# Kernel tuning notes

Hardware: AMD Instinct MI355X
Metric: run time of the kernel (lower is better)

The kernel has to match this reference:

```python
import jax, jax.numpy as jnp
import numpy as np

N_NODES = 100000
EPS = 1e-07


def _gconv(src, dst, x, W, b):
    # DGL GraphConv with norm='both': D_dst^{-1/2} A (D_src^{-1/2} x) W + b
    ones = jnp.ones(src.shape[0], x.dtype)
    deg_out = jax.ops.segment_sum(ones, src, num_segments=N_NODES)
    deg_in = jax.ops.segment_sum(ones, dst, num_segments=N_NODES)
    norm_out = jnp.where(deg_out > 0, deg_out, 1.0) ** -0.5
    norm_in = jnp.where(deg_in > 0, deg_in, 1.0) ** -0.5
    h = x * norm_out[:, None]
    agg = jax.ops.segment_sum(h[src], dst, num_segments=N_NODES)  # [N, d]
    agg = agg * norm_in[:, None]
    return agg @ W + b


def _branch(npemb, gauss, unif, temp, Wm, bm, Wl, bl, Wq, bq, Wd1, bd1, WdX, bdX, Wc, bc):
    cat = unif.shape[-1]
    mean = npemb @ Wm + bm                      # [E, d_z]
    logstd = npemb @ Wl + bl                    # [E, d_z]
    Nlat = gauss * jnp.exp(logstd) + mean       # reparameterization
    Nlat = Nlat.reshape(npemb.shape[0], cat, -1)  # [E, cat, d_m]
    q = npemb @ Wq + bq                         # [E, cat]
    gumbel = -jnp.log(-jnp.log(unif + EPS) + EPS)
    Z = jax.nn.softmax((q + gumbel) / temp, axis=-1)  # [E, cat]
    M = jnp.einsum('ec,ecd->ed', Z, Nlat)       # [E, d_m]
    X = jax.nn.relu(jax.nn.relu(M @ Wd1 + bd1) @ WdX + bdX)
    A = jax.nn.softmax(M @ Wc + bc, axis=-1)
    return A, X, mean, logstd, q


def setup_inputs() -> dict:
    key = jax.random.key(0)
    ks = jax.random.split(key, 32)
    E_g, E = 800000, 262144
    d_in, d_h, d_z, cat, d_m, d_dec, d_out = 128, 256, 256, 4, 64, 256, 128
    s = 0.05
    inp = {
        'x': jax.random.normal(ks[0], (N_NODES, d_in), jnp.float32),
        'src': jax.random.randint(ks[1], (E_g,), 0, N_NODES),
        'dst': jax.random.randint(ks[2], (E_g,), 0, N_NODES),
        'pos_src': jax.random.randint(ks[3], (E,), 0, N_NODES),
        'pos_dst': jax.random.randint(ks[4], (E,), 0, N_NODES),
        'neg_src': jax.random.randint(ks[5], (E,), 0, N_NODES),
        'neg_dst': jax.random.randint(ks[6], (E,), 0, N_NODES),
        'gauss_pos': jax.random.normal(ks[7], (E, d_z), jnp.float32),
        'gauss_neg': jax.random.normal(ks[8], (E, d_z), jnp.float32),
        'unif_pos': jax.random.uniform(ks[9], (E, cat), jnp.float32),
        'unif_neg': jax.random.uniform(ks[10], (E, cat), jnp.float32),
        'temp': 1,
        'W1': jax.random.normal(ks[11], (d_in, d_h), jnp.float32) * s,
        'b1': jnp.zeros((d_h,), jnp.float32),
        'W2': jax.random.normal(ks[12], (d_h, d_h), jnp.float32) * s,
        'b2': jnp.zeros((d_h,), jnp.float32),
        'Wm': jax.random.normal(ks[13], (d_h, d_z), jnp.float32) * s,
        'bm': jnp.zeros((d_z,), jnp.float32),
        'Wl': jax.random.normal(ks[14], (d_h, d_z), jnp.float32) * s,
        'bl': jnp.zeros((d_z,), jnp.float32),
        'Wq': jax.random.normal(ks[15], (d_h, cat), jnp.float32) * s,
        'bq': jnp.zeros((cat,), jnp.float32),
        'Wd1': jax.random.normal(ks[16], (d_m, d_dec), jnp.float32) * s,
        'bd1': jnp.zeros((d_dec,), jnp.float32),
        'WdX': jax.random.normal(ks[17], (d_dec, d_out), jnp.float32) * s,
        'bdX': jnp.zeros((d_out,), jnp.float32),
        'Wc': jax.random.normal(ks[18], (d_m, cat), jnp.float32) * s,
        'bc': jnp.zeros((cat,), jnp.float32),
    }
    return inp


def reference(x, src, dst, pos_src, pos_dst, neg_src, neg_dst,
              gauss_pos, gauss_neg, unif_pos, unif_neg, temp,
              W1, b1, W2, b2, Wm, bm, Wl, bl, Wq, bq,
              Wd1, bd1, WdX, bdX, Wc, bc):
    # two-layer GraphConv encoder (relu after layer 0; dropout in eval mode = identity)
    h = jax.nn.relu(_gconv(src, dst, x, W1, b1))
    h = _gconv(src, dst, h, W2, b2)
    # u_add_v edge gather
    pos_npemb = h[pos_src] + h[pos_dst]
    neg_npemb = h[neg_src] + h[neg_dst]
    t = jnp.asarray(temp, h.dtype)
    posA, posX, pos_mean, pos_logstd, posq = _branch(
        pos_npemb, gauss_pos, unif_pos, t, Wm, bm, Wl, bl, Wq, bq, Wd1, bd1, WdX, bdX, Wc, bc)
    negA, negX, neg_mean, neg_logstd, negq = _branch(
        neg_npemb, gauss_neg, unif_neg, t, Wm, bm, Wl, bl, Wq, bq, Wd1, bd1, WdX, bdX, Wc, bc)
    return (posA, negA, posX, negX, pos_mean, neg_mean,
            pos_logstd, neg_logstd, posq, negq)
```

## Files before the change

kernel.cpp:

```cpp
#include <hip/hip_runtime.h>
#include <hip/hip_bf16.h>


#define NN 100000
#define EG 800000
#define EE 262144
#define NB 98

typedef __attribute__((ext_vector_type(8))) short short8;
typedef __attribute__((ext_vector_type(4))) float f32x4;
typedef __attribute__((ext_vector_type(2))) float f32x2;

__device__ __forceinline__ float lo2f(unsigned u) {
  union { unsigned u; float f; } v; v.u = u << 16; return v.f;
}
__device__ __forceinline__ float hi2f(unsigned u) {
  union { unsigned u; float f; } v; v.u = u & 0xFFFF0000u; return v.f;
}
__device__ __forceinline__ unsigned short f2bf(float f) {
  union { float f; unsigned u; } v; v.f = f;
  return (unsigned short)((v.u + 0x7FFFu + ((v.u >> 16) & 1u)) >> 16);
}
__device__ __forceinline__ unsigned pack2bf(float a, float b) {
  return (unsigned)f2bf(a) | ((unsigned)f2bf(b) << 16);
}
__device__ __forceinline__ int permc(int c) {
  return (c & ~31) | ((c & 15) << 1) | ((c >> 4) & 1);
}

__device__ __forceinline__ float decode_scalar(const void* p) {
  unsigned u = *(const unsigned*)p;
  float f = __uint_as_float(u);
  float af = fabsf(f);
  if (af >= 1e-6f && af <= 1e6f) return f;
  if (u < 1024u) return (float)u;
  return 1.0f;
}

__global__ __launch_bounds__(256) void k_deg(const int* __restrict__ src,
                                             const int* __restrict__ dst,
                                             int* __restrict__ degO,
                                             int* __restrict__ degI) {
  for (int i = blockIdx.x * 256 + threadIdx.x; i < EG; i += gridDim.x * 256) {
    atomicAdd(&degO[src[i]], 1);
    atomicAdd(&degI[dst[i]], 1);
  }
}

__global__ __launch_bounds__(1024) void k_scan1(const int* __restrict__ degI,
                                                int* __restrict__ rowptr,
                                                int* __restrict__ bsum) {
  __shared__ int wsum[16];
  int t = threadIdx.x, lane = t & 63, wv = t >> 6;
  int i = blockIdx.x * 1024 + t;
  int v = (i < NN) ? degI[i] : 0;
  int incl = v;
#pragma unroll
  for (int off = 1; off < 64; off <<= 1) {
    int u = __shfl_up(incl, off);
    if (lane >= off) incl += u;
  }
  if (lane == 63) wsum[wv] = incl;
  __syncthreads();
  if (wv == 0 && lane < 16) {
    int s = wsum[lane];
    int si = s;
#pragma unroll
    for (int off = 1; off < 16; off <<= 1) {
      int u = __shfl_up(si, off);
      if (lane >= off) si += u;
    }
    wsum[lane] = si - s;
    if (lane == 15) bsum[blockIdx.x] = si;
  }
  __syncthreads();
  int excl = wsum[wv] + incl - v;
  if (i < NN) rowptr[i] = excl;
}

__global__ __launch_bounds__(128) void k_scan2(int* __restrict__ bsum) {
  __shared__ int w0tot;
  int t = threadIdx.x, lane = t & 63, wv = t >> 6;
  int v = (t < NB) ? bsum[t] : 0;
  int incl = v;
#pragma unroll
  for (int off = 1; off < 64; off <<= 1) {
    int u = __shfl_up(incl, off);
    if (lane >= off) incl += u;
  }
  if (wv == 0 && lane == 63) w0tot = incl;
  __syncthreads();
  int excl = incl - v + (wv ? w0tot : 0);
  if (t < NB) bsum[t] = excl;
}

__global__ __launch_bounds__(1024) void k_scan3(const int* __restrict__ degI,
                                                const int* __restrict__ degO,
                                                int* __restrict__ rowptr,
                                                int* __restrict__ cursor,
                                                const int* __restrict__ bsum,
                                                float* __restrict__ normO,
                                                float* __restrict__ normI) {
  int i = blockIdx.x * 1024 + threadIdx.x;
  if (i < NN) {
    int vv = rowptr[i] + bsum[blockIdx.x];
    rowptr[i] = vv;
    cursor[i] = vv;
    if (i == NN - 1) rowptr[NN] = vv + degI[i];
    int dO = degO[i]; if (dO < 1) dO = 1;
    int dI = degI[i]; if (dI < 1) dI = 1;
    normO[i] = rsqrtf((float)dO);
    normI[i] = rsqrtf((float)dI);
  }
}

__global__ __launch_bounds__(256) void k_fill(const int* __restrict__ src,
                                              const int* __restrict__ dst,
                                              int* __restrict__ cursor,
                                              int* __restrict__ csr) {
  for (int e = blockIdx.x * 256 + threadIdx.x; e < EG; e += gridDim.x * 256) {
    int d = dst[e];
    int pos = atomicAdd(&cursor[d], 1);
    csr[pos] = src[e];
  }
}

__global__ __launch_bounds__(256) void k_transpose_all(
    const float* __restrict__ W1, const float* __restrict__ W2,
    const float* __restrict__ Wm, const float* __restrict__ Wl,
    const float* __restrict__ Wd1, const float* __restrict__ WdX,
    const float* __restrict__ Wq,
    unsigned short* __restrict__ W1T, unsigned short* __restrict__ W2T,
    unsigned short* __restrict__ WmT, unsigned short* __restrict__ WlT,
    unsigned short* __restrict__ Wd1T, unsigned short* __restrict__ WdXT,
    unsigned short* __restrict__ WqT) {
  int idx = blockIdx.x * 256 + threadIdx.x;
  if (idx < 32768) {
    int n = idx & 255, k = idx >> 8;
    W1T[n * 128 + k] = f2bf(W1[idx]);
  } else if (idx < 98304) {
    int i = idx - 32768;
    int n = i & 255, k = i >> 8;
    W2T[n * 256 + k] = f2bf(W2[i]);
  } else if (idx < 163840) {
    int i = idx - 98304;
    int n = i & 255, k = i >> 8;
    WmT[n * 256 + k] = f2bf(Wm[i]);
  } else if (idx < 229376) {
    int i = idx - 163840;
    int n = i & 255, k = i >> 8;
    WlT[n * 256 + k] = f2bf(Wl[i]);
  } else if (idx < 245760) {
    int i = idx - 229376;
    int n = i & 255, k = i >> 8;
    Wd1T[n * 64 + k] = f2bf(Wd1[i]);
  } else if (idx < 278528) {
    int i = idx - 245760;
    int n = i & 127, k = i >> 7;
    WdXT[n * 256 + k] = f2bf(WdX[i]);
  } else if (idx < 282624) {
    int i = idx - 278528;
    int r = i >> 8, k = i & 255;
    WqT[i] = (r < 4) ? f2bf(Wq[k * 4 + r]) : (unsigned short)0;
  }
}

__global__ __launch_bounds__(256) void k_gather1(
    const float* __restrict__ x, const int* __restrict__ rowptr,
    const int* __restrict__ csr, const float* __restrict__ normO,
    const float* __restrict__ normI, unsigned short* __restrict__ agg) {
  int wid = (blockIdx.x * 256 + threadIdx.x) >> 6;
  int lane = threadIdx.x & 63;
  int half = lane >> 5, fl = lane & 31;
  int nw = (gridDim.x * 256) >> 6;
  for (int n = wid; n < NN; n += nw) {
    int beg = rowptr[n], end = rowptr[n + 1];
    float a0 = 0.f, a1 = 0.f, a2 = 0.f, a3 = 0.f;
    float b0 = 0.f, b1 = 0.f, b2 = 0.f, b3 = 0.f;
    int i = beg + half;
    for (; i + 2 < end; i += 4) {
      int s0 = csr[i], s1 = csr[i + 2];
      float ns0 = normO[s0], ns1 = normO[s1];
      float4 v0 = *(const float4*)(x + ((size_t)s0 << 7) + (fl << 2));
      float4 v1 = *(const float4*)(x + ((size_t)s1 << 7) + (fl << 2));
      a0 += ns0 * v0.x; a1 += ns0 * v0.y; a2 += ns0 * v0.z; a3 += ns0 * v0.w;
      b0 += ns1 * v1.x; b1 += ns1 * v1.y; b2 += ns1 * v1.z; b3 += ns1 * v1.w;
    }
    for (; i < end; i += 2) {
      int s0 = csr[i];
      float ns0 = normO[s0];
      float4 v0 = *(const float4*)(x + ((size_t)s0 << 7) + (fl << 2));
      a0 += ns0 * v0.x; a1 += ns0 * v0.y; a2 += ns0 * v0.z; a3 += ns0 * v0.w;
    }
    a0 += b0; a1 += b1; a2 += b2; a3 += b3;
    a0 += __shfl_xor(a0, 32); a1 += __shfl_xor(a1, 32);
    a2 += __shfl_xor(a2, 32); a3 += __shfl_xor(a3, 32);
    if (lane < 32) {
      float ni = normI[n];
      *(uint2*)(agg + ((size_t)n << 7) + (fl << 2)) =
          make_uint2(pack2bf(a0 * ni, a1 * ni), pack2bf(a2 * ni, a3 * ni));
    }
  }
}

__global__ __launch_bounds__(256) void k_gather2(
    const unsigned short* __restrict__ h1s, const int* __restrict__ rowptr,
    const int* __restrict__ csr, const float* __restrict__ normI,
    unsigned short* __restrict__ agg) {
  int wid = (blockIdx.x * 256 + threadIdx.x) >> 6;
  int lane = threadIdx.x & 63;
  int half = lane >> 5, fl = lane & 31;
  int nw = (gridDim.x * 256) >> 6;
  for (int n = wid; n < NN; n += nw) {
    int beg = rowptr[n], end = rowptr[n + 1];
    float a0 = 0.f, a1 = 0.f, a2 = 0.f, a3 = 0.f, a4 = 0.f, a5 = 0.f, a6 = 0.f, a7 = 0.f;
    float c0 = 0.f, c1 = 0.f, c2 = 0.f, c3 = 0.f, c4 = 0.f, c5 = 0.f, c6 = 0.f, c7 = 0.f;
    int i = beg + half;
    for (; i + 2 < end; i += 4) {
      int s0 = csr[i], s1 = csr[i + 2];
      uint4 v = *(const uint4*)(h1s + ((size_t)s0 << 8) + (fl << 3));
      uint4 u = *(const uint4*)(h1s + ((size_t)s1 << 8) + (fl << 3));
      a0 += lo2f(v.x); a1 += hi2f(v.x);
      a2 += lo2f(v.y); a3 += hi2f(v.y);
      a4 += lo2f(v.z); a5 += hi2f(v.z);
      a6 += lo2f(v.w); a7 += hi2f(v.w);
      c0 += lo2f(u.x); c1 += hi2f(u.x);
      c2 += lo2f(u.y); c3 += hi2f(u.y);
      c4 += lo2f(u.z); c5 += hi2f(u.z);
      c6 += lo2f(u.w); c7 += hi2f(u.w);
    }
    for (; i < end; i += 2) {
      int s0 = csr[i];
      uint4 v = *(const uint4*)(h1s + ((size_t)s0 << 8) + (fl << 3));
      a0 += lo2f(v.x); a1 += hi2f(v.x);
      a2 += lo2f(v.y); a3 += hi2f(v.y);
      a4 += lo2f(v.z); a5 += hi2f(v.z);
      a6 += lo2f(v.w); a7 += hi2f(v.w);
    }
    a0 += c0; a1 += c1; a2 += c2; a3 += c3;
    a4 += c4; a5 += c5; a6 += c6; a7 += c7;
    a0 += __shfl_xor(a0, 32); a1 += __shfl_xor(a1, 32);
    a2 += __shfl_xor(a2, 32); a3 += __shfl_xor(a3, 32);
    a4 += __shfl_xor(a4, 32); a5 += __shfl_xor(a5, 32);
    a6 += __shfl_xor(a6, 32); a7 += __shfl_xor(a7, 32);
    if (lane < 32) {
      float ni = normI[n];
      uint4 o;
      o.x = pack2bf(a0 * ni, a1 * ni);
      o.y = pack2bf(a2 * ni, a3 * ni);
      o.z = pack2bf(a4 * ni, a5 * ni);
      o.w = pack2bf(a6 * ni, a7 * ni);
      *(uint4*)(agg + ((size_t)n << 8) + (fl << 3)) = o;
    }
  }
}

template <int K, bool RELU, bool OSCALE>
__global__ __launch_bounds__(256) void k_gemm(
    const unsigned short* __restrict__ A, const float* __restrict__ oscale,
    const unsigned short* __restrict__ WT, const float* __restrict__ bias,
    unsigned short* __restrict__ C, int M) {
  __shared__ __align__(16) short At[128 * 40];
  __shared__ __align__(16) short Bt[256 * 40];
  const int t = threadIdx.x;
  const int row0 = blockIdx.x * 128;
  const int lane = t & 63, wave = t >> 6;
  const int wr = (wave >> 1) << 6;
  const int wcc = (wave & 1) << 7;
  const int lrow = lane & 15, lhi = lane >> 4;

  f32x4 acc[4][8];
#pragma unroll
  for (int m = 0; m < 4; ++m)
#pragma unroll
    for (int n = 0; n < 8; ++n) acc[m][n] = (f32x4){0.f, 0.f, 0.f, 0.f};

  for (int k0 = 0; k0 < K; k0 += 32) {
    if (k0) __syncthreads();
#pragma unroll
    for (int it = 0; it < 2; ++it) {
      int idx = t + it * 256;
      int r = idx >> 2, c8 = (idx & 3) << 3;
      int grow = row0 + r;
      int4 tv = {0, 0, 0, 0};
      if (grow < M) tv = *(const int4*)(A + (size_t)grow * K + k0 + c8);
      *(int4*)&At[r * 40 + c8] = tv;
    }
    {
      const unsigned short* wt = WT + (size_t)permc(t) * K + k0;
      *(int4*)&Bt[t * 40 + 0] = *(const int4*)(wt);
      *(int4*)&Bt[t * 40 + 8] = *(const int4*)(wt + 8);
      *(int4*)&Bt[t * 40 + 16] = *(const int4*)(wt + 16);
      *(int4*)&Bt[t * 40 + 24] = *(const int4*)(wt + 24);
    }
    __syncthreads();
    short8 a[4], b[8];
#pragma unroll
    for (int m = 0; m < 4; ++m)
      a[m] = *(const short8*)&At[(wr + m * 16 + lrow) * 40 + lhi * 8];
#pragma unroll
    for (int n = 0; n < 8; ++n)
      b[n] = *(const short8*)&Bt[(wcc + n * 16 + lrow) * 40 + lhi * 8];
#pragma unroll
    for (int m = 0; m < 4; ++m)
#pragma unroll
      for (int n = 0; n < 8; ++n)
        acc[m][n] = __builtin_amdgcn_mfma_f32_16x16x32_bf16(a[m], b[n], acc[m][n], 0, 0, 0);
  }
#pragma unroll
  for (int np = 0; np < 4; ++np) {
    int tc = wcc + np * 32 + (lrow << 1);
    float bv0 = bias[tc], bv1 = bias[tc + 1];
#pragma unroll
    for (int m = 0; m < 4; ++m) {
#pragma unroll
      for (int r = 0; r < 4; ++r) {
        int grow = row0 + wr + m * 16 + lhi * 4 + r;
        if (grow < M) {
          float v0 = acc[m][2 * np][r] + bv0;
          float v1 = acc[m][2 * np + 1][r] + bv1;
          if (RELU) { v0 = fmaxf(v0, 0.f); v1 = fmaxf(v1, 0.f); }
          if (OSCALE) { float s = oscale[grow]; v0 *= s; v1 *= s; }
          *(unsigned*)&C[(size_t)grow * 256 + tc] = pack2bf(v0, v1);
        }
      }
    }
  }
}

__global__ __launch_bounds__(512) void k_branch2(
    const unsigned short* __restrict__ h, const int* __restrict__ ea,
    const int* __restrict__ eb, const float* __restrict__ gauss,
    const float* __restrict__ unif, const void* __restrict__ temp_p,
    const unsigned short* __restrict__ WmT, const float* __restrict__ bm,
    const unsigned short* __restrict__ WlT, const float* __restrict__ bl,
    const unsigned short* __restrict__ WqT, const float* __restrict__ bq,
    const float* __restrict__ Wc, const float* __restrict__ bc,
    float* __restrict__ o_mean, float* __restrict__ o_ls,
    float* __restrict__ q_o, float* __restrict__ A_o,
    unsigned* __restrict__ M_o32) {
  __shared__ __align__(16) char U[33792];
  short* At = (short*)U;
  float* Mf = (float*)U;
  __shared__ float zS[512];
  __shared__ float qS[512];
  __shared__ float WcT[4 * 68];
  __shared__ float bmS[256], blS[256];
  __shared__ int eaS[128], ebS[128];

  const int t = threadIdx.x;
  const int e0 = blockIdx.x << 7;
  const int lane = t & 63;
  const int wv = t >> 6;
  const int lrow = lane & 15, lhi = lane >> 4;
  const int wc = wv << 5;

  if (t < 256) {
    bmS[t] = bm[t]; blS[t] = bl[t];
    WcT[(t & 3) * 68 + (t >> 2)] = Wc[t];
  } else if (t < 384) {
    eaS[t - 256] = ea[e0 + t - 256];
  } else {
    ebS[t - 384] = eb[e0 + t - 384];
  }
  __syncthreads();

  f32x4 am[8][2], al[8][2], aq;
#pragma unroll
  for (int m = 0; m < 8; ++m)
#pragma unroll
    for (int n = 0; n < 2; ++n) {
      am[m][n] = (f32x4){0.f, 0.f, 0.f, 0.f};
      al[m][n] = (f32x4){0.f, 0.f, 0.f, 0.f};
    }
  aq = (f32x4){0.f, 0.f, 0.f, 0.f};

  const int ar = t >> 2, as_ = t & 3;
  const int arsw = ((as_ ^ (ar & 3)) << 3);
  const int fsw = (lrow & 3);

  const unsigned short* pa_base = h + ((size_t)eaS[ar] << 8) + (as_ << 3);
  const unsigned short* pb_base = h + ((size_t)ebS[ar] << 8) + (as_ << 3);
  const size_t row0p = (size_t)permc(wc + lrow) << 8;
  const size_t row1p = (size_t)permc(wc + 16 + lrow) << 8;
  const unsigned short* bm0p = WmT + row0p + (lhi << 3);
  const unsigned short* bm1p = WmT + row1p + (lhi << 3);
  const unsigned short* bl0p = WlT + row0p + (lhi << 3);
  const unsigned short* bl1p = WlT + row1p + (lhi << 3);
  const unsigned short* bqp = WqT + ((size_t)lrow << 8) + (lhi << 3);

  uint4 va = *(const uint4*)pa_base;
  uint4 vb = *(const uint4*)pb_base;

  for (int k0 = 0; k0 < 256; k0 += 32) {
    unsigned w0 = pack2bf(lo2f(va.x) + lo2f(vb.x), hi2f(va.x) + hi2f(vb.x));
    unsigned w1 = pack2bf(lo2f(va.y) + lo2f(vb.y), hi2f(va.y) + hi2f(vb.y));
    unsigned w2 = pack2bf(lo2f(va.z) + lo2f(vb.z), hi2f(va.z) + hi2f(vb.z));
    unsigned w3 = pack2bf(lo2f(va.w) + lo2f(vb.w), hi2f(va.w) + hi2f(vb.w));
    if (k0 < 224) {
      va = *(const uint4*)(pa_base + k0 + 32);
      vb = *(const uint4*)(pb_base + k0 + 32);
    }
    short8 bmf0 = *(const short8*)(bm0p + k0);
    short8 bmf1 = *(const short8*)(bm1p + k0);
    short8 blf0 = *(const short8*)(bl0p + k0);
    short8 blf1 = *(const short8*)(bl1p + k0);
    short8 bqf = *(const short8*)(bqp + k0);
    if (k0) __syncthreads();
    *(int4*)&At[ar * 32 + arsw] = make_int4((int)w0, (int)w1, (int)w2, (int)w3);
    __syncthreads();
    short8 a[8], aqa;
#pragma unroll
    for (int m = 0; m < 8; ++m)
      a[m] = *(const short8*)&At[(m * 16 + lrow) * 32 + ((lhi ^ fsw) << 3)];
    aqa = *(const short8*)&At[((wv << 4) + lrow) * 32 + ((lhi ^ fsw) << 3)];
#pragma unroll
    for (int m = 0; m < 8; ++m) {
      am[m][0] = __builtin_amdgcn_mfma_f32_16x16x32_bf16(a[m], bmf0, am[m][0], 0, 0, 0);
      am[m][1] = __builtin_amdgcn_mfma_f32_16x16x32_bf16(a[m], bmf1, am[m][1], 0, 0, 0);
      al[m][0] = __builtin_amdgcn_mfma_f32_16x16x32_bf16(a[m], blf0, al[m][0], 0, 0, 0);
      al[m][1] = __builtin_amdgcn_mfma_f32_16x16x32_bf16(a[m], blf1, al[m][1], 0, 0, 0);
    }
    aq = __builtin_amdgcn_mfma_f32_16x16x32_bf16(aqa, bqf, aq, 0, 0, 0);
  }
  __syncthreads();

  float invt = 1.0f / decode_scalar(temp_p);
  float qb = (lrow < 4) ? bq[lrow] : 0.f;
#pragma unroll
  for (int r = 0; r < 4; ++r) {
    int el = (wv << 4) + lhi * 4 + r;
    float q = aq[r] + qb;
    float uu = 0.5f;
    if (lrow < 4) uu = unif[(((size_t)(e0 + el)) << 2) + lrow];
    float g = -__logf(-__logf(uu + 1e-7f) + 1e-7f);
    float z = (q + g) * invt;
    float mx = fmaxf(z, __shfl_xor(z, 1));
    mx = fmaxf(mx, __shfl_xor(mx, 2));
    float ez = __expf(z - mx);
    float sz = ez + __shfl_xor(ez, 1);
    sz += __shfl_xor(sz, 2);
    if (lrow < 4) { zS[el * 4 + lrow] = ez / sz; qS[el * 4 + lrow] = q; }
  }
  for (int i = t; i < 128 * 66; i += 512) Mf[i] = 0.f;
  __syncthreads();

  __builtin_nontemporal_store(qS[t], q_o + (((size_t)e0) << 2) + t);

  const int cidx = wv >> 1;
  const int dd = ((wv & 1) << 5) + (lrow << 1);
  const int tc = wc + (lrow << 1);
  float bm0 = bmS[tc], bm1 = bmS[tc + 1];
  float bl0 = blS[tc], bl1 = blS[tc + 1];
#pragma unroll
  for (int m = 0; m < 8; ++m) {
#pragma unroll
    for (int r = 0; r < 4; ++r) {
      int row = m * 16 + lhi * 4 + r;
      size_t gi = (((size_t)(e0 + row)) << 8) + tc;
      float mv0 = am[m][0][r] + bm0, mv1 = am[m][1][r] + bm1;
      float lv0 = al[m][0][r] + bl0, lv1 = al[m][1][r] + bl1;
      __builtin_nontemporal_store((f32x2){mv0, mv1}, (f32x2*)(o_mean + gi));
      __builtin_nontemporal_store((f32x2){lv0, lv1}, (f32x2*)(o_ls + gi));
      f32x2 g2 = __builtin_nontemporal_load((const f32x2*)(gauss + gi));
      float zc = zS[(row << 2) + cidx];
      atomicAdd(&Mf[row * 66 + dd], zc * (g2.x * __expf(lv0) + mv0));
      atomicAdd(&Mf[row * 66 + dd + 1], zc * (g2.y * __expf(lv1) + mv1));
    }
  }
  __syncthreads();

  {
    int e = t >> 2, cat = t & 3;
    const float* mrow = &Mf[e * 66];
    const float* wct = &WcT[cat * 68];
    float s = 0.f;
#pragma unroll
    for (int dp = 0; dp < 32; ++dp) {
      float2 m2 = *(const float2*)(mrow + 2 * dp);
      s += m2.x * wct[2 * dp] + m2.y * wct[2 * dp + 1];
    }
    s += bc[cat];
    float smx = fmaxf(s, __shfl_xor(s, 1));
    smx = fmaxf(smx, __shfl_xor(smx, 2));
    float es = __expf(s - smx);
    float ssum = es + __shfl_xor(es, 1);
    ssum += __shfl_xor(ssum, 2);
    __builtin_nontemporal_store(es / ssum, A_o + (((size_t)e0) << 2) + t);
  }
#pragma unroll
  for (int j = 0; j < 8; ++j) {
    int idx = j * 512 + t;
    int row = idx >> 5, dp = idx & 31;
    float2 m2 = *(const float2*)(&Mf[row * 66 + 2 * dp]);
    M_o32[((size_t)(e0 + row)) * 32 + dp] = pack2bf(m2.x, m2.y);
  }
}

__global__ __launch_bounds__(512) void k_dec2(
    const unsigned short* __restrict__ Mw, const unsigned short* __restrict__ Wd1T,
    const float* __restrict__ bd1, const unsigned short* __restrict__ WdXT,
    const float* __restrict__ bdX, float* __restrict__ Xo) {
  __shared__ __align__(16) char R[65280];
  short* Mt = (short*)R;
  short* Bt1 = (short*)(R + 9216);
  short* X1 = (short*)R;
  short* Bt2 = (short*)(R + 46848);
  const int t = threadIdx.x, lane = t & 63, wv = t >> 6;
  const int lrow = lane & 15, lhi = lane >> 4;
  const int e0 = blockIdx.x << 6;

  const int r2 = t >> 2, base2 = (t & 3) << 4;
  const unsigned short* wpb = WdXT + ((size_t)permc(r2) << 8) + base2;

  {
    int r = t >> 3, c8 = (t & 7) << 3;
    *(int4*)&Mt[r * 72 + c8] = *(const int4*)(Mw + (((size_t)(e0 + r)) << 6) + c8);
  }
  {
    int r1 = t >> 1, base = (t & 1) << 5;
    const unsigned short* wp = Wd1T + ((size_t)permc(r1) << 6) + base;
#pragma unroll
    for (int j = 0; j < 4; ++j)
      *(int4*)&Bt1[r1 * 72 + base + j * 8] = *(const int4*)(wp + j * 8);
  }
  int4 pw0 = *(const int4*)(wpb);
  int4 pw1 = *(const int4*)(wpb + 8);
  __syncthreads();
  f32x4 acc1[4][2];
#pragma unroll
  for (int m = 0; m < 4; ++m)
#pragma unroll
    for (int n = 0; n < 2; ++n) acc1[m][n] = (f32x4){0.f, 0.f, 0.f, 0.f};
  const int wc1 = wv << 5;
  {
    short8 a0[4], a1[4], b0[2], b1[2];
#pragma unroll
    for (int m = 0; m < 4; ++m) {
      a0[m] = *(const short8*)&Mt[(m * 16 + lrow) * 72 + lhi * 8];
      a1[m] = *(const short8*)&Mt[(m * 16 + lrow) * 72 + 32 + lhi * 8];
    }
#pragma unroll
    for (int n = 0; n < 2; ++n) {
      b0[n] = *(const short8*)&Bt1[(wc1 + n * 16 + lrow) * 72 + lhi * 8];
      b1[n] = *(const short8*)&Bt1[(wc1 + n * 16 + lrow) * 72 + 32 + lhi * 8];
    }
#pragma unroll
    for (int m = 0; m < 4; ++m)
#pragma unroll
      for (int n = 0; n < 2; ++n) {
        acc1[m][n] = __builtin_amdgcn_mfma_f32_16x16x32_bf16(a0[m], b0[n], acc1[m][n], 0, 0, 0);
        acc1[m][n] = __builtin_amdgcn_mfma_f32_16x16x32_bf16(a1[m], b1[n], acc1[m][n], 0, 0, 0);
      }
  }
  __syncthreads();
  {
    int tc = wc1 + (lrow << 1);
    float bdv0 = bd1[tc], bdv1 = bd1[tc + 1];
#pragma unroll
    for (int m = 0; m < 4; ++m)
#pragma unroll
      for (int r = 0; r < 4; ++r) {
        int row = m * 16 + lhi * 4 + r;
        float v0 = fmaxf(acc1[m][0][r] + bdv0, 0.f);
        float v1 = fmaxf(acc1[m][1][r] + bdv1, 0.f);
        *(unsigned*)&X1[row * 264 + tc] = pack2bf(v0, v1);
      }
  }

  f32x4 acc2[2][2];
#pragma unroll
  for (int m = 0; m < 2; ++m)
#pragma unroll
    for (int n = 0; n < 2; ++n) acc2[m][n] = (f32x4){0.f, 0.f, 0.f, 0.f};
  const int wr2 = (wv >> 2) << 5, wc2 = (wv & 3) << 5;
  for (int k0 = 0; k0 < 256; k0 += 64) {
    __syncthreads();
    *(int4*)&Bt2[r2 * 72 + base2] = pw0;
    *(int4*)&Bt2[r2 * 72 + base2 + 8] = pw1;
    if (k0 < 192) {
      pw0 = *(const int4*)(wpb + k0 + 64);
      pw1 = *(const int4*)(wpb + k0 + 64 + 8);
    }
    __syncthreads();
    short8 c0[2], c1[2], d0[2], d1[2];
#pragma unroll
    for (int m = 0; m < 2; ++m) {
      c0[m] = *(const short8*)&X1[(wr2 + m * 16 + lrow) * 264 + k0 + lhi * 8];
      c1[m] = *(const short8*)&X1[(wr2 + m * 16 + lrow) * 264 + k0 + 32 + lhi * 8];
    }
#pragma unroll
    for (int n = 0; n < 2; ++n) {
      d0[n] = *(const short8*)&Bt2[(wc2 + n * 16 + lrow) * 72 + lhi * 8];
      d1[n] = *(const short8*)&Bt2[(wc2 + n * 16 + lrow) * 72 + 32 + lhi * 8];
    }
#pragma unroll
    for (int m = 0; m < 2; ++m)
#pragma unroll
      for (int n = 0; n < 2; ++n) {
        acc2[m][n] = __builtin_amdgcn_mfma_f32_16x16x32_bf16(c0[m], d0[n], acc2[m][n], 0, 0, 0);
        acc2[m][n] = __builtin_amdgcn_mfma_f32_16x16x32_bf16(c1[m], d1[n], acc2[m][n], 0, 0, 0);
      }
  }
  {
    int tc2 = wc2 + (lrow << 1);
    float bx0 = bdX[tc2], bx1 = bdX[tc2 + 1];
#pragma unroll
    for (int m = 0; m < 2; ++m)
#pragma unroll
      for (int r = 0; r < 4; ++r) {
        int row = wr2 + m * 16 + lhi * 4 + r;
        float v0 = fmaxf(acc2[m][0][r] + bx0, 0.f);
        float v1 = fmaxf(acc2[m][1][r] + bx1, 0.f);
        __builtin_nontemporal_store((f32x2){v0, v1},
                                    (f32x2*)(Xo + (((size_t)(e0 + row)) << 7) + tc2));
      }
  }
}

extern "C" void kernel_launch(void* const* d_in, const int* in_sizes, int n_in,
                              void* d_out, int out_size, void* d_ws, size_t ws_size,
                              hipStream_t stream) {
  const float* x = (const float*)d_in[0];
  const int* src = (const int*)d_in[1];
  const int* dst = (const int*)d_in[2];
  const int* pos_src = (const int*)d_in[3];
  const int* pos_dst = (const int*)d_in[4];
  const int* neg_src = (const int*)d_in[5];
  const int* neg_dst = (const int*)d_in[6];
  const float* gauss_pos = (const float*)d_in[7];
  const float* gauss_neg = (const float*)d_in[8];
  const float* unif_pos = (const float*)d_in[9];
  const float* unif_neg = (const float*)d_in[10];
  const void* temp_p = d_in[11];
  const float* W1 = (const float*)d_in[12];
  const float* b1 = (const float*)d_in[13];
  const float* W2 = (const float*)d_in[14];
  const float* b2 = (const float*)d_in[15];
  const float* Wm = (const float*)d_in[16];
  const float* bm = (const float*)d_in[17];
  const float* Wl = (const float*)d_in[18];
  const float* bl = (const float*)d_in[19];
  const float* Wq = (const float*)d_in[20];
  const float* bq = (const float*)d_in[21];
  const float* Wd1 = (const float*)d_in[22];
  const float* bd1 = (const float*)d_in[23];
  const float* WdX = (const float*)d_in[24];
  const float* bdX = (const float*)d_in[25];
  const float* Wc = (const float*)d_in[26];
  const float* bc = (const float*)d_in[27];

  char* w = (char*)d_ws;
  int* degO = (int*)w;
  int* degI = (int*)(w + 401408);
  int* rowptr = (int*)(w + 802816);
  int* cursor = (int*)(w + 1204224);
  float* normO = (float*)(w + 1605632);
  float* normI = (float*)(w + 2007040);
  int* csr = (int*)(w + 2408448);
  unsigned short* W1T = (unsigned short*)(w + 5609472);
  unsigned short* W2T = (unsigned short*)(w + 5675008);
  unsigned short* WmT = (unsigned short*)(w + 5806080);
  unsigned short* WlT = (unsigned short*)(w + 5937152);
  unsigned short* Wd1T = (unsigned short*)(w + 6068224);
  unsigned short* WdXT = (unsigned short*)(w + 6100992);
  unsigned short* WqT = (unsigned short*)(w + 6166528);
  int* bsum = (int*)(w + 6174720);
  unsigned short* agg1 = (unsigned short*)(w + 6175232);
  unsigned short* h1s = (unsigned short*)(w + 31775232);
  unsigned short* agg2 = (unsigned short*)(w + 82975232);
  unsigned short* h = (unsigned short*)(w + 134175232);
  unsigned short* Mws = (unsigned short*)(w + 185375232);

  float* out = (float*)d_out;
  float* posA = out;
  float* negA = out + 1048576ull;
  float* posX = out + 2097152ull;
  float* negX = out + 35651584ull;
  float* pos_mean = out + 69206016ull;
  float* neg_mean = out + 136314880ull;
  float* pos_logstd = out + 203423744ull;
  float* neg_logstd = out + 270532608ull;
  float* posq = out + 337641472ull;
  float* negq = out + 338690048ull;

  hipMemsetAsync(d_ws, 0, 802816, stream);

  k_deg<<<1024, 256, 0, stream>>>(src, dst, degO, degI);
  k_scan1<<<NB, 1024, 0, stream>>>(degI, rowptr, bsum);
  k_scan2<<<1, 128, 0, stream>>>(bsum);
  k_scan3<<<NB, 1024, 0, stream>>>(degI, degO, rowptr, cursor, bsum, normO, normI);
  k_fill<<<2048, 256, 0, stream>>>(src, dst, cursor, csr);
  k_transpose_all<<<1104, 256, 0, stream>>>(W1, W2, Wm, Wl, Wd1, WdX, Wq,
                                            W1T, W2T, WmT, WlT, Wd1T, WdXT, WqT);

  k_gather1<<<2048, 256, 0, stream>>>(x, rowptr, csr, normO, normI, agg1);
  k_gemm<128, true, true><<<782, 256, 0, stream>>>(agg1, normO, W1T, b1, h1s, NN);
  k_gather2<<<2048, 256, 0, stream>>>(h1s, rowptr, csr, normI, agg2);
  k_gemm<256, false, false><<<782, 256, 0, stream>>>(agg2, nullptr, W2T, b2, h, NN);

  for (int b = 0; b < 2; ++b) {
    const int* es = b ? neg_src : pos_src;
    const int* ed = b ? neg_dst : pos_dst;
    const float* gs = b ? gauss_neg : gauss_pos;
    const float* uf = b ? unif_neg : unif_pos;
    float* o_mean = b ? neg_mean : pos_mean;
    float* o_ls = b ? neg_logstd : pos_logstd;
    float* o_q = b ? negq : posq;
    float* o_A = b ? negA : posA;
    float* o_X = b ? negX : posX;

    k_branch2<<<2048, 512, 0, stream>>>(h, es, ed, gs, uf, temp_p,
                                        WmT, bm, WlT, bl, WqT, bq, Wc, bc,
                                        o_mean, o_ls, o_q, o_A, (unsigned*)Mws);
    k_dec2<<<4096, 512, 0, stream>>>(Mws, Wd1T, bd1, WdXT, bdX, o_X);
  }
}
```

Before: 1.375 ms.

## Gather layer-1 features from a bf16 copy of x and stream decoder weights from global

```diff
diff --git a/kernel.cpp b/kernel.cpp
--- a/kernel.cpp
+++ b/kernel.cpp
@@ -122,6 +122,15 @@
     int d = dst[e];
     int pos = atomicAdd(&cursor[d], 1);
     csr[pos] = src[e];
+  }
+}
+
+__global__ __launch_bounds__(256) void k_xbf16(const float* __restrict__ x,
+                                               unsigned short* __restrict__ xb) {
+  int i = blockIdx.x * 256 + threadIdx.x;
+  if (i < NN * 32) {
+    float4 v = *(const float4*)(x + (size_t)i * 4);
+    *(uint2*)(xb + (size_t)i * 4) = make_uint2(pack2bf(v.x, v.y), pack2bf(v.z, v.w));
   }
 }
 
@@ -166,7 +175,7 @@
 }
 
 __global__ __launch_bounds__(256) void k_gather1(
-    const float* __restrict__ x, const int* __restrict__ rowptr,
+    const unsigned short* __restrict__ xb, const int* __restrict__ rowptr,
     const int* __restrict__ csr, const float* __restrict__ normO,
     const float* __restrict__ normI, unsigned short* __restrict__ agg) {
   int wid = (blockIdx.x * 256 + threadIdx.x) >> 6;
@@ -181,16 +190,19 @@
     for (; i + 2 < end; i += 4) {
       int s0 = csr[i], s1 = csr[i + 2];
       float ns0 = normO[s0], ns1 = normO[s1];
-      float4 v0 = *(const float4*)(x + ((size_t)s0 << 7) + (fl << 2));
-      float4 v1 = *(const float4*)(x + ((size_t)s1 << 7) + (fl << 2));
-      a0 += ns0 * v0.x; a1 += ns0 * v0.y; a2 += ns0 * v0.z; a3 += ns0 * v0.w;
-      b0 += ns1 * v1.x; b1 += ns1 * v1.y; b2 += ns1 * v1.z; b3 += ns1 * v1.w;
+      uint2 v0 = *(const uint2*)(xb + ((size_t)s0 << 7) + (fl << 2));
+      uint2 v1 = *(const uint2*)(xb + ((size_t)s1 << 7) + (fl << 2));
+      a0 += ns0 * lo2f(v0.x); a1 += ns0 * hi2f(v0.x);
+      a2 += ns0 * lo2f(v0.y); a3 += ns0 * hi2f(v0.y);
+      b0 += ns1 * lo2f(v1.x); b1 += ns1 * hi2f(v1.x);
+      b2 += ns1 * lo2f(v1.y); b3 += ns1 * hi2f(v1.y);
     }
     for (; i < end; i += 2) {
       int s0 = csr[i];
       float ns0 = normO[s0];
-      float4 v0 = *(const float4*)(x + ((size_t)s0 << 7) + (fl << 2));
-      a0 += ns0 * v0.x; a1 += ns0 * v0.y; a2 += ns0 * v0.z; a3 += ns0 * v0.w;
+      uint2 v0 = *(const uint2*)(xb + ((size_t)s0 << 7) + (fl << 2));
+      a0 += ns0 * lo2f(v0.x); a1 += ns0 * hi2f(v0.x);
+      a2 += ns0 * lo2f(v0.y); a3 += ns0 * hi2f(v0.y);
     }
     a0 += b0; a1 += b1; a2 += b2; a3 += b3;
     a0 += __shfl_xor(a0, 32); a1 += __shfl_xor(a1, 32);
@@ -501,60 +513,34 @@
     const unsigned short* __restrict__ Mw, const unsigned short* __restrict__ Wd1T,
     const float* __restrict__ bd1, const unsigned short* __restrict__ WdXT,
     const float* __restrict__ bdX, float* __restrict__ Xo) {
-  __shared__ __align__(16) char R[65280];
-  short* Mt = (short*)R;
-  short* Bt1 = (short*)(R + 9216);
-  short* X1 = (short*)R;
-  short* Bt2 = (short*)(R + 46848);
+  __shared__ __align__(16) short X1[64 * 264];
   const int t = threadIdx.x, lane = t & 63, wv = t >> 6;
   const int lrow = lane & 15, lhi = lane >> 4;
   const int e0 = blockIdx.x << 6;
 
-  const int r2 = t >> 2, base2 = (t & 3) << 4;
-  const unsigned short* wpb = WdXT + ((size_t)permc(r2) << 8) + base2;
-
-  {
-    int r = t >> 3, c8 = (t & 7) << 3;
-    *(int4*)&Mt[r * 72 + c8] = *(const int4*)(Mw + (((size_t)(e0 + r)) << 6) + c8);
-  }
-  {
-    int r1 = t >> 1, base = (t & 1) << 5;
-    const unsigned short* wp = Wd1T + ((size_t)permc(r1) << 6) + base;
-#pragma unroll
-    for (int j = 0; j < 4; ++j)
-      *(int4*)&Bt1[r1 * 72 + base + j * 8] = *(const int4*)(wp + j * 8);
-  }
-  int4 pw0 = *(const int4*)(wpb);
-  int4 pw1 = *(const int4*)(wpb + 8);
-  __syncthreads();
-  f32x4 acc1[4][2];
-#pragma unroll
-  for (int m = 0; m < 4; ++m)
-#pragma unroll
-    for (int n = 0; n < 2; ++n) acc1[m][n] = (f32x4){0.f, 0.f, 0.f, 0.f};
   const int wc1 = wv << 5;
   {
-    short8 a0[4], a1[4], b0[2], b1[2];
+    f32x4 acc1[4][2];
+#pragma unroll
+    for (int m = 0; m < 4; ++m)
+#pragma unroll
+      for (int n = 0; n < 2; ++n) acc1[m][n] = (f32x4){0.f, 0.f, 0.f, 0.f};
+    const unsigned short* b0p = Wd1T + ((size_t)permc(wc1 + lrow) << 6) + (lhi << 3);
+    const unsigned short* b1p = Wd1T + ((size_t)permc(wc1 + 16 + lrow) << 6) + (lhi << 3);
+    short8 b00 = *(const short8*)(b0p);
+    short8 b01 = *(const short8*)(b0p + 32);
+    short8 b10 = *(const short8*)(b1p);
+    short8 b11 = *(const short8*)(b1p + 32);
 #pragma unroll
     for (int m = 0; m < 4; ++m) {
-      a0[m] = *(const short8*)&Mt[(m * 16 + lrow) * 72 + lhi * 8];
-      a1[m] = *(const short8*)&Mt[(m * 16 + lrow) * 72 + 32 + lhi * 8];
-    }
-#pragma unroll
-    for (int n = 0; n < 2; ++n) {
-      b0[n] = *(const short8*)&Bt1[(wc1 + n * 16 + lrow) * 72 + lhi * 8];
-      b1[n] = *(const short8*)&Bt1[(wc1 + n * 16 + lrow) * 72 + 32 + lhi * 8];
-    }
-#pragma unroll
-    for (int m = 0; m < 4; ++m)
-#pragma unroll
-      for (int n = 0; n < 2; ++n) {
-        acc1[m][n] = __builtin_amdgcn_mfma_f32_16x16x32_bf16(a0[m], b0[n], acc1[m][n], 0, 0, 0);
-        acc1[m][n] = __builtin_amdgcn_mfma_f32_16x16x32_bf16(a1[m], b1[n], acc1[m][n], 0, 0, 0);
-      }
-  }
-  __syncthreads();
-  {
+      const unsigned short* ap = Mw + (((size_t)(e0 + m * 16 + lrow)) << 6) + (lhi << 3);
+      short8 a0 = *(const short8*)(ap);
+      short8 a1 = *(const short8*)(ap + 32);
+      acc1[m][0] = __builtin_amdgcn_mfma_f32_16x16x32_bf16(a0, b00, acc1[m][0], 0, 0, 0);
+      acc1[m][1] = __builtin_amdgcn_mfma_f32_16x16x32_bf16(a0, b10, acc1[m][1], 0, 0, 0);
+      acc1[m][0] = __builtin_amdgcn_mfma_f32_16x16x32_bf16(a1, b01, acc1[m][0], 0, 0, 0);
+      acc1[m][1] = __builtin_amdgcn_mfma_f32_16x16x32_bf16(a1, b11, acc1[m][1], 0, 0, 0);
+    }
     int tc = wc1 + (lrow << 1);
     float bdv0 = bd1[tc], bdv1 = bd1[tc + 1];
 #pragma unroll
@@ -567,6 +553,7 @@
         *(unsigned*)&X1[row * 264 + tc] = pack2bf(v0, v1);
       }
   }
+  __syncthreads();
 
   f32x4 acc2[2][2];
 #pragma unroll
@@ -574,33 +561,18 @@
 #pragma unroll
     for (int n = 0; n < 2; ++n) acc2[m][n] = (f32x4){0.f, 0.f, 0.f, 0.f};
   const int wr2 = (wv >> 2) << 5, wc2 = (wv & 3) << 5;
-  for (int k0 = 0; k0 < 256; k0 += 64) {
-    __syncthreads();
-    *(int4*)&Bt2[r2 * 72 + base2] = pw0;
-    *(int4*)&Bt2[r2 * 72 + base2 + 8] = pw1;
-    if (k0 < 192) {
-      pw0 = *(const int4*)(wpb + k0 + 64);
-      pw1 = *(const int4*)(wpb + k0 + 64 + 8);
-    }
-    __syncthreads();
-    short8 c0[2], c1[2], d0[2], d1[2];
-#pragma unroll
-    for (int m = 0; m < 2; ++m) {
-      c0[m] = *(const short8*)&X1[(wr2 + m * 16 + lrow) * 264 + k0 + lhi * 8];
-      c1[m] = *(const short8*)&X1[(wr2 + m * 16 + lrow) * 264 + k0 + 32 + lhi * 8];
-    }
-#pragma unroll
-    for (int n = 0; n < 2; ++n) {
-      d0[n] = *(const short8*)&Bt2[(wc2 + n * 16 + lrow) * 72 + lhi * 8];
-      d1[n] = *(const short8*)&Bt2[(wc2 + n * 16 + lrow) * 72 + 32 + lhi * 8];
-    }
-#pragma unroll
-    for (int m = 0; m < 2; ++m)
-#pragma unroll
-      for (int n = 0; n < 2; ++n) {
-        acc2[m][n] = __builtin_amdgcn_mfma_f32_16x16x32_bf16(c0[m], d0[n], acc2[m][n], 0, 0, 0);
-        acc2[m][n] = __builtin_amdgcn_mfma_f32_16x16x32_bf16(c1[m], d1[n], acc2[m][n], 0, 0, 0);
-      }
+  const unsigned short* d0p = WdXT + ((size_t)permc(wc2 + lrow) << 8) + (lhi << 3);
+  const unsigned short* d1p = WdXT + ((size_t)permc(wc2 + 16 + lrow) << 8) + (lhi << 3);
+#pragma unroll
+  for (int k0 = 0; k0 < 256; k0 += 32) {
+    short8 d0 = *(const short8*)(d0p + k0);
+    short8 d1 = *(const short8*)(d1p + k0);
+    short8 c0 = *(const short8*)&X1[(wr2 + lrow) * 264 + k0 + lhi * 8];
+    short8 c1 = *(const short8*)&X1[(wr2 + 16 + lrow) * 264 + k0 + lhi * 8];
+    acc2[0][0] = __builtin_amdgcn_mfma_f32_16x16x32_bf16(c0, d0, acc2[0][0], 0, 0, 0);
+    acc2[0][1] = __builtin_amdgcn_mfma_f32_16x16x32_bf16(c0, d1, acc2[0][1], 0, 0, 0);
+    acc2[1][0] = __builtin_amdgcn_mfma_f32_16x16x32_bf16(c1, d0, acc2[1][0], 0, 0, 0);
+    acc2[1][1] = __builtin_amdgcn_mfma_f32_16x16x32_bf16(c1, d1, acc2[1][1], 0, 0, 0);
   }
   {
     int tc2 = wc2 + (lrow << 1);
@@ -671,6 +643,7 @@
   unsigned short* agg2 = (unsigned short*)(w + 82975232);
   unsigned short* h = (unsigned short*)(w + 134175232);
   unsigned short* Mws = (unsigned short*)(w + 185375232);
+  unsigned short* xb = (unsigned short*)(w + 218929664);
 
   float* out = (float*)d_out;
   float* posA = out;
@@ -691,10 +664,11 @@
   k_scan2<<<1, 128, 0, stream>>>(bsum);
   k_scan3<<<NB, 1024, 0, stream>>>(degI, degO, rowptr, cursor, bsum, normO, normI);
   k_fill<<<2048, 256, 0, stream>>>(src, dst, cursor, csr);
+  k_xbf16<<<12500, 256, 0, stream>>>(x, xb);
   k_transpose_all<<<1104, 256, 0, stream>>>(W1, W2, Wm, Wl, Wd1, WdX, Wq,
                                             W1T, W2T, WmT, WlT, Wd1T, WdXT, WqT);
 
-  k_gather1<<<2048, 256, 0, stream>>>(x, rowptr, csr, normO, normI, agg1);
+  k_gather1<<<2048, 256, 0, stream>>>(xb, rowptr, csr, normO, normI, agg1);
   k_gemm<128, true, true><<<782, 256, 0, stream>>>(agg1, normO, W1T, b1, h1s, NN);
   k_gather2<<<2048, 256, 0, stream>>>(h1s, rowptr, csr, normI, agg2);
   k_gemm<256, false, false><<<782, 256, 0, stream>>>(agg2, nullptr, W2T, b2, h, NN);
```

After: 1.477 ms. +7.4%, slower.
